# Optimization experiments

Measured on AMD Instinct MI355X. Metric: run time of the kernel, lower is better.

The kernel has to match this reference:

```python
import jax, jax.numpy as jnp
import numpy as np

N, M, BS = 32, 64, 512
ALPHA, BETA = 1.0, 1.0


def setup_inputs() -> dict:
    key = jax.random.key(0)
    k1, k2, k3, k4 = jax.random.split(key, 4)
    q = jax.random.normal(k1, (BS, N), jnp.float32)
    b = jax.random.normal(k2, (BS, M), jnp.float32)
    A0 = jax.random.normal(k3, (N, N), jnp.float32)
    P = A0 @ A0.T / N + jnp.eye(N, dtype=jnp.float32)  # SPD cost matrix
    H = jax.random.normal(k4, (M, N), jnp.float32) / jnp.sqrt(jnp.float32(N))
    return {"q": q, "b": b, "P": P, "H": H, "iters": 1000}


def reference(q, b, P, H, iters):
    m = H.shape[0]
    # Pinv-applied quantities via solve (matches torch.linalg.solve / pinv usage)
    Pinv_q = jnp.linalg.solve(P, q.T).T                 # (bs, n)
    D = H @ jnp.linalg.solve(P, H.T)                    # (m, m) = H P^-1 H^T
    # dummy preconditioner: scaled identity keeping the operator nonexpansive
    lam_max = jnp.linalg.eigvalsh(D)[-1]
    tD = (BETA / lam_max) * jnp.eye(m, dtype=q.dtype)   # (m, m)
    mu = ((H @ Pinv_q.T).T - b) @ tD.T                  # (bs, m)
    tDD = tD @ D
    I = jnp.eye(m, dtype=q.dtype)
    A = jnp.block([[tDD, tD],
                   [-2.0 * ALPHA * tDD + I, I - 2.0 * ALPHA * tD]])  # (2m, 2m)
    B = jnp.concatenate([mu, -2.0 * ALPHA * mu], axis=1)             # (bs, 2m)
    Hinv = jnp.linalg.pinv(H)                            # (n, m)
    X0 = jnp.zeros((q.shape[0], 2 * m), q.dtype)

    def step(X, _):
        X = X @ A.T + B
        X = X.at[:, m:].set(jax.nn.relu(X[:, m:]))       # in-place ReLU on dual half
        return X, X

    _, ys = jax.lax.scan(step, X0, None, length=iters)   # (iters, bs, 2m)
    Xs = jnp.concatenate([X0[None], ys], axis=0).transpose(1, 0, 2)  # (bs, iters+1, 2m)
    # primal_sols[k] = Hinv @ (X_k[m:] - b)
    primal_sols = jnp.einsum('nm,bkm->bkn', Hinv, Xs[:, :, m:] - b[:, None, :])
    return Xs, primal_sols
```

## Files before the change

kernel.cpp:

```cpp
#include <hip/hip_runtime.h>
#include <math.h>

#define BATCH 512
#define ITERS 1000
#define PHASES 125

typedef float f32x2 __attribute__((ext_vector_type(2)));
typedef float f32x4 __attribute__((ext_vector_type(4)));

__device__ __forceinline__ float rdlane(float v, int l) {
  return __int_as_float(__builtin_amdgcn_readlane(__float_as_int(v), l));
}
__device__ __forceinline__ f32x2 fma2(f32x2 a, f32x2 b, f32x2 c) {
#if __has_builtin(__builtin_elementwise_fma)
  return __builtin_elementwise_fma(a, b, c);
#else
  f32x2 r; r.x = fmaf(a.x, b.x, c.x); r.y = fmaf(a.y, b.y, c.y); return r;
#endif
}

#define GJ32_REG(g)                                            \
  _Pragma("unroll")                                            \
  for (int k = 0; k < 32; ++k) {                               \
    float inv = 1.0f / rdlane(g[k], k);                        \
    g[k] *= inv;                                               \
    _Pragma("unroll")                                          \
    for (int ii = 0; ii < 32; ++ii) {                          \
      if (ii == k) continue;                                   \
      float f = rdlane(g[ii], k);                              \
      g[ii] = fmaf(-f, g[k], g[ii]);                           \
    }                                                          \
  }

__global__ __launch_bounds__(128, 1)
void fused_kernel(const float* __restrict__ q,
                  const float* __restrict__ bmat,
                  const float* __restrict__ P,
                  const float* __restrict__ H,
                  float* __restrict__ Xs,
                  float* __restrict__ out2) {
  __shared__ __align__(16) float stage[2112];
  __shared__ __align__(16) float ring[2][8][64];

  const int tid = threadIdx.x;
  const int wv = tid >> 6;
  const int lane = tid & 63;
  const int row = blockIdx.x;
  const int i = lane & 31, h = lane >> 5;

  float hreg[32];
  {
    const f32x4* hp = (const f32x4*)(H + lane * 32);
    #pragma unroll
    for (int j4 = 0; j4 < 8; ++j4) {
      f32x4 t = hp[j4];
      hreg[4*j4+0] = t.x; hreg[4*j4+1] = t.y; hreg[4*j4+2] = t.z; hreg[4*j4+3] = t.w;
    }
  }
  const float bl = bmat[row * 64 + lane];

  float dcol[64]; float s = 0.f, mu = 0.f;
  f32x2 hv2[16];
  float* Xp = Xs + (size_t)row * (ITERS + 1) * 128;
  float* ob = out2 + (size_t)row * (ITERS + 1) * 32;

  if (wv == 1) {
    #pragma unroll
    for (int j = 0; j < 32; ++j) stage[lane * 33 + j] = hreg[j];
  }
  __syncthreads();
  float gB[32];
  if (wv == 1) {
    float htc[64];
    #pragma unroll
    for (int m = 0; m < 64; ++m) htc[m] = stage[m * 33 + i];
    #pragma unroll
    for (int r = 0; r < 32; ++r) {
      float a0 = 0.f, a1 = 0.f;
      #pragma unroll
      for (int m = 0; m < 64; m += 2) {
        a0 = fmaf(rdlane(hreg[r], m),     htc[m],     a0);
        a1 = fmaf(rdlane(hreg[r], m + 1), htc[m + 1], a1);
      }
      float hth = a0 + a1;
      gB[r] = (lane < 32) ? hth : (((lane - 32) == r) ? 1.0f : 0.0f);
    }
    GJ32_REG(gB)
  }
  __syncthreads();
  if (wv == 1) {
    #pragma unroll
    for (int r = 0; r < 32; ++r) {
      float a0 = 0.f, a1 = 0.f;
      #pragma unroll
      for (int c = 0; c < 32; c += 2) {
        a0 = fmaf(rdlane(gB[r], 32 + c),     hreg[c],     a0);
        a1 = fmaf(rdlane(gB[r], 32 + c + 1), hreg[c + 1], a1);
      }
      stage[r * 66 + lane] = a0 + a1;
    }
  }
  __syncthreads();
  if (wv == 1) {
    #pragma unroll
    for (int t = 0; t < 16; ++t)
      hv2[t] = *(const f32x2*)&stage[i * 66 + 32 * h + 2 * t];
  }

  if (wv == 0) {
    float pht[32], acc;
    {
      float g[32];
      #pragma unroll
      for (int r = 0; r < 32; ++r) {
        float pv = P[r * 32 + i];
        g[r] = (lane < 32) ? pv : (((lane - 32) == r) ? 1.0f : 0.0f);
      }
      GJ32_REG(g)
      #pragma unroll
      for (int r = 0; r < 32; ++r) {
        float a0 = 0.f, a1 = 0.f;
        #pragma unroll
        for (int j = 0; j < 32; j += 2) {
          a0 = fmaf(rdlane(g[r], 32 + j),     hreg[j],     a0);
          a1 = fmaf(rdlane(g[r], 32 + j + 1), hreg[j + 1], a1);
        }
        pht[r] = a0 + a1;
      }
    }
    {
      const float* qp = q + row * 32;
      float a0 = 0.f, a1 = 0.f;
      #pragma unroll
      for (int r = 0; r < 32; r += 2) {
        a0 = fmaf(qp[r],     pht[r],     a0);
        a1 = fmaf(qp[r + 1], pht[r + 1], a1);
      }
      acc = a0 + a1;
    }
    #pragma unroll
    for (int r = 0; r < 64; ++r) {
      float a0 = 0.f, a1 = 0.f;
      #pragma unroll
      for (int j = 0; j < 32; j += 2) {
        a0 = fmaf(rdlane(hreg[j],     r), pht[j],     a0);
        a1 = fmaf(rdlane(hreg[j + 1], r), pht[j + 1], a1);
      }
      dcol[r] = a0 + a1;
    }
    {
      float ecol[64];
      #pragma unroll
      for (int r = 0; r < 64; ++r) {
        float a0 = 0.f, a1 = 0.f;
        #pragma unroll
        for (int c = 0; c < 64; c += 2) {
          a0 = fmaf(rdlane(dcol[r], c),     dcol[c],     a0);
          a1 = fmaf(rdlane(dcol[r], c + 1), dcol[c + 1], a1);
        }
        ecol[r] = a0 + a1;
      }
      float v = 1.0f + 0.017f * (float)lane;
      #pragma unroll 1
      for (int t = 0; t < 112; ++t) {
        float a0 = 0.f, a1 = 0.f, a2 = 0.f, a3 = 0.f;
        #pragma unroll
        for (int c = 0; c < 64; c += 4) {
          a0 = fmaf(ecol[c+0], rdlane(v, c+0), a0);
          a1 = fmaf(ecol[c+1], rdlane(v, c+1), a1);
          a2 = fmaf(ecol[c+2], rdlane(v, c+2), a2);
          a3 = fmaf(ecol[c+3], rdlane(v, c+3), a3);
        }
        v = (a0 + a1) + (a2 + a3);
        if ((t & 7) == 7) {
          float n2 = v * v;
          #pragma unroll
          for (int m = 1; m < 64; m <<= 1) n2 += __shfl_xor(n2, m);
          v *= 1.0f / sqrtf(n2);
        }
      }
      float a0 = 0.f, a1 = 0.f, a2 = 0.f, a3 = 0.f;
      #pragma unroll
      for (int c = 0; c < 64; c += 4) {
        a0 = fmaf(dcol[c+0], rdlane(v, c+0), a0);
        a1 = fmaf(dcol[c+1], rdlane(v, c+1), a1);
        a2 = fmaf(dcol[c+2], rdlane(v, c+2), a2);
        a3 = fmaf(dcol[c+3], rdlane(v, c+3), a3);
      }
      float w = (a0 + a1) + (a2 + a3);
      float num = w * v, den = v * v;
      #pragma unroll
      for (int m = 1; m < 64; m <<= 1) {
        num += __shfl_xor(num, m);
        den += __shfl_xor(den, m);
      }
      s = den / num;
    }
    mu = s * (acc - bl);
    #pragma unroll
    for (int r = 0; r < 64; ++r) dcol[r] *= s;
    Xp[lane] = 0.f;
    Xp[64 + lane] = 0.f;
  }

  float x1 = 0.f, x2 = 0.f;
  #pragma unroll 1
  for (int p = 0; p < PHASES; ++p) {
    if (wv == 0) {
      float* rb = &ring[p & 1][0][0];
      #pragma unroll
      for (int u = 0; u < 8; ++u) {
        float a0 = 0.f, a1 = 0.f, a2 = 0.f, a3 = 0.f;
        #pragma unroll
        for (int j = 0; j < 64; j += 4) {
          a0 = fmaf(dcol[j+0], rdlane(x1, j+0), a0);
          a1 = fmaf(dcol[j+1], rdlane(x1, j+1), a1);
          a2 = fmaf(dcol[j+2], rdlane(x1, j+2), a2);
          a3 = fmaf(dcol[j+3], rdlane(x1, j+3), a3);
        }
        float x1n = ((a0 + a1) + (a2 + a3)) + fmaf(s, x2, mu);
        float x2n = fmaxf(fmaf(-2.0f, x1n, x1 + x2), 0.f);
        Xp += 128;
        Xp[lane] = x1n;
        Xp[64 + lane] = x2n;
        rb[u * 64 + lane] = x2n - bl;
        x1 = x1n; x2 = x2n;
      }
    } else {
      if (p == 0) {
        f32x2 pa = {0.f, 0.f}, pb = {0.f, 0.f};
        #pragma unroll
        for (int t = 0; t < 8; ++t) {
          f32x2 ta, tb;
          ta.x = -__shfl(bl, 32*h + 4*t + 0, 64);
          ta.y = -__shfl(bl, 32*h + 4*t + 1, 64);
          tb.x = -__shfl(bl, 32*h + 4*t + 2, 64);
          tb.y = -__shfl(bl, 32*h + 4*t + 3, 64);
          pa = fma2(hv2[2*t],     ta, pa);
          pb = fma2(hv2[2*t + 1], tb, pb);
        }
        float pr = (pa.x + pa.y) + (pb.x + pb.y);
        pr += __shfl_xor(pr, 32);
        if (h == 0) ob[i] = pr;
      } else {
        const float* rbuf = &ring[(p - 1) & 1][0][0];
        #pragma unroll
        for (int u = 0; u < 8; ++u) {
          const int k = 8 * (p - 1) + 1 + u;
          const f32x4* tp = (const f32x4*)(rbuf + u * 64 + h * 32);
          f32x2 pa = {0.f, 0.f}, pb = {0.f, 0.f};
          #pragma unroll
          for (int t = 0; t < 8; ++t) {
            f32x4 tv = tp[t];
            pa = fma2(hv2[2*t],     tv.xy, pa);
            pb = fma2(hv2[2*t + 1], tv.zw, pb);
          }
          float pr = (pa.x + pa.y) + (pb.x + pb.y);
          pr += __shfl_xor(pr, 32);
          if (h == 0) ob[(size_t)k * 32 + i] = pr;
        }
      }
    }
    __syncthreads();
  }

  if (wv == 1) {
    const float* rbuf = &ring[0][0][0];
    #pragma unroll
    for (int u = 0; u < 8; ++u) {
      const int k = 993 + u;
      const f32x4* tp = (const f32x4*)(rbuf + u * 64 + h * 32);
      f32x2 pa = {0.f, 0.f}, pb = {0.f, 0.f};
      #pragma unroll
      for (int t = 0; t < 8; ++t) {
        f32x4 tv = tp[t];
        pa = fma2(hv2[2*t],     tv.xy, pa);
        pb = fma2(hv2[2*t + 1], tv.zw, pb);
      }
      float pr = (pa.x + pa.y) + (pb.x + pb.y);
      pr += __shfl_xor(pr, 32);
      if (h == 0) ob[(size_t)k * 32 + i] = pr;
    }
  }
}

extern "C" void kernel_launch(void* const* d_in, const int* in_sizes, int n_in,
                              void* d_out, int out_size, void* d_ws, size_t ws_size,
                              hipStream_t stream) {
  (void)in_sizes; (void)n_in; (void)out_size; (void)d_ws; (void)ws_size;
  const float* q = (const float*)d_in[0];
  const float* b = (const float*)d_in[1];
  const float* P = (const float*)d_in[2];
  const float* H = (const float*)d_in[3];
  float* Xs = (float*)d_out;
  float* out2 = Xs + (size_t)BATCH * (ITERS + 1) * 128;

  fused_kernel<<<BATCH, 128, 0, stream>>>(q, b, P, H, Xs, out2);
}
```

Before: 615.6 us.

## Offload Xs global stores to consumer wave and lengthen pipeline phases

After: 611.9 us. No clear change (-0.6%).

```diff
diff --git a/kernel.cpp b/kernel.cpp
--- a/kernel.cpp
+++ b/kernel.cpp
@@ -3,7 +3,8 @@
 
 #define BATCH 512
 #define ITERS 1000
-#define PHASES 125
+#define PLEN 25
+#define PHASES 40
 
 typedef float f32x2 __attribute__((ext_vector_type(2)));
 typedef float f32x4 __attribute__((ext_vector_type(4)));
@@ -40,7 +41,8 @@
                   float* __restrict__ Xs,
                   float* __restrict__ out2) {
   __shared__ __align__(16) float stage[2112];
-  __shared__ __align__(16) float ring[2][8][64];
+  __shared__ __align__(16) float X1R[2][PLEN][64];
+  __shared__ __align__(16) float X2R[2][PLEN][64];
 
   const int tid = threadIdx.x;
   const int wv = tid >> 6;
@@ -199,35 +201,42 @@
     mu = s * (acc - bl);
     #pragma unroll
     for (int r = 0; r < 64; ++r) dcol[r] *= s;
-    Xp[lane] = 0.f;
-    Xp[64 + lane] = 0.f;
   }
 
   float x1 = 0.f, x2 = 0.f;
   #pragma unroll 1
   for (int p = 0; p < PHASES; ++p) {
     if (wv == 0) {
-      float* rb = &ring[p & 1][0][0];
-      #pragma unroll
-      for (int u = 0; u < 8; ++u) {
+      float* rx1 = &X1R[p & 1][0][0];
+      float* rx2 = &X2R[p & 1][0][0];
+      #pragma unroll 1
+      for (int u = 0; u < PLEN; ++u) {
         float a0 = 0.f, a1 = 0.f, a2 = 0.f, a3 = 0.f;
         #pragma unroll
-        for (int j = 0; j < 64; j += 4) {
-          a0 = fmaf(dcol[j+0], rdlane(x1, j+0), a0);
-          a1 = fmaf(dcol[j+1], rdlane(x1, j+1), a1);
-          a2 = fmaf(dcol[j+2], rdlane(x1, j+2), a2);
-          a3 = fmaf(dcol[j+3], rdlane(x1, j+3), a3);
+        for (int j8 = 0; j8 < 64; j8 += 8) {
+          float b0 = rdlane(x1, j8+0), b1 = rdlane(x1, j8+1);
+          float b2 = rdlane(x1, j8+2), b3 = rdlane(x1, j8+3);
+          float b4 = rdlane(x1, j8+4), b5 = rdlane(x1, j8+5);
+          float b6 = rdlane(x1, j8+6), b7 = rdlane(x1, j8+7);
+          a0 = fmaf(dcol[j8+0], b0, a0);
+          a1 = fmaf(dcol[j8+1], b1, a1);
+          a2 = fmaf(dcol[j8+2], b2, a2);
+          a3 = fmaf(dcol[j8+3], b3, a3);
+          a0 = fmaf(dcol[j8+4], b4, a0);
+          a1 = fmaf(dcol[j8+5], b5, a1);
+          a2 = fmaf(dcol[j8+6], b6, a2);
+          a3 = fmaf(dcol[j8+7], b7, a3);
         }
         float x1n = ((a0 + a1) + (a2 + a3)) + fmaf(s, x2, mu);
         float x2n = fmaxf(fmaf(-2.0f, x1n, x1 + x2), 0.f);
-        Xp += 128;
-        Xp[lane] = x1n;
-        Xp[64 + lane] = x2n;
-        rb[u * 64 + lane] = x2n - bl;
+        rx1[u * 64 + lane] = x1n;
+        rx2[u * 64 + lane] = x2n - bl;
         x1 = x1n; x2 = x2n;
       }
     } else {
       if (p == 0) {
+        Xp[lane] = 0.f;
+        Xp[64 + lane] = 0.f;
         f32x2 pa = {0.f, 0.f}, pb = {0.f, 0.f};
         #pragma unroll
         for (int t = 0; t < 8; ++t) {
@@ -243,11 +252,18 @@
         pr += __shfl_xor(pr, 32);
         if (h == 0) ob[i] = pr;
       } else {
-        const float* rbuf = &ring[(p - 1) & 1][0][0];
-        #pragma unroll
-        for (int u = 0; u < 8; ++u) {
-          const int k = 8 * (p - 1) + 1 + u;
-          const f32x4* tp = (const f32x4*)(rbuf + u * 64 + h * 32);
+        const float* rx1 = &X1R[(p - 1) & 1][0][0];
+        const float* rx2 = &X2R[(p - 1) & 1][0][0];
+        const int k0 = PLEN * (p - 1) + 1;
+        float* Xk = Xp + (size_t)k0 * 128;
+        float* obk = ob + (size_t)k0 * 32;
+        #pragma unroll 1
+        for (int u = 0; u < PLEN; ++u) {
+          float x1v = rx1[u * 64 + lane];
+          float x2mb = rx2[u * 64 + lane];
+          Xk[u * 128 + lane] = x1v;
+          Xk[u * 128 + 64 + lane] = x2mb + bl;
+          const f32x4* tp = (const f32x4*)(rx2 + u * 64 + h * 32);
           f32x2 pa = {0.f, 0.f}, pb = {0.f, 0.f};
           #pragma unroll
           for (int t = 0; t < 8; ++t) {
@@ -257,7 +273,7 @@
           }
           float pr = (pa.x + pa.y) + (pb.x + pb.y);
           pr += __shfl_xor(pr, 32);
-          if (h == 0) ob[(size_t)k * 32 + i] = pr;
+          if (h == 0) obk[u * 32 + i] = pr;
         }
       }
     }
@@ -265,11 +281,18 @@
   }
 
   if (wv == 1) {
-    const float* rbuf = &ring[0][0][0];
-    #pragma unroll
-    for (int u = 0; u < 8; ++u) {
-      const int k = 993 + u;
-      const f32x4* tp = (const f32x4*)(rbuf + u * 64 + h * 32);
+    const float* rx1 = &X1R[1][0][0];
+    const float* rx2 = &X2R[1][0][0];
+    const int k0 = PLEN * (PHASES - 1) + 1;
+    float* Xk = Xp + (size_t)k0 * 128;
+    float* obk = ob + (size_t)k0 * 32;
+    #pragma unroll 1
+    for (int u = 0; u < PLEN; ++u) {
+      float x1v = rx1[u * 64 + lane];
+      float x2mb = rx2[u * 64 + lane];
+      Xk[u * 128 + lane] = x1v;
+      Xk[u * 128 + 64 + lane] = x2mb + bl;
+      const f32x4* tp = (const f32x4*)(rx2 + u * 64 + h * 32);
       f32x2 pa = {0.f, 0.f}, pb = {0.f, 0.f};
       #pragma unroll
       for (int t = 0; t < 8; ++t) {
@@ -279,7 +302,7 @@
       }
       float pr = (pa.x + pa.y) + (pb.x + pb.y);
       pr += __shfl_xor(pr, 32);
-      if (h == 0) ob[(size_t)k * 32 + i] = pr;
+      if (h == 0) obk[u * 32 + i] = pr;
     }
   }
 }
```
